# Kernel optimization log

Measured on AMD Instinct MI355X. Metric: run time of the kernel, lower is better.

Reference implementation:

```python
import jax, jax.numpy as jnp
import numpy as np

B, T, QD, AD = 64, 2048, 1024, 256


def setup_inputs() -> dict:
    key = jax.random.key(0)
    k1, k2, k3, k4, k5 = jax.random.split(key, 5)
    encoder_seq_proj = jax.random.normal(k1, (B, T, AD), dtype=jnp.float32)
    query = jax.random.normal(k2, (B, QD), dtype=jnp.float32)
    chars = jax.random.randint(k3, (B, T), 0, 60, dtype=jnp.int64)
    # learned params (nn.Linear, bias=False): weight shape (out, in)
    Wq = jax.random.normal(k4, (AD, QD), dtype=jnp.float32) / np.sqrt(QD)
    v = jax.random.normal(k5, (AD,), dtype=jnp.float32) / np.sqrt(AD)
    return {"encoder_seq_proj": encoder_seq_proj, "query": query,
            "chars": chars, "t": 1, "Wq": Wq, "v": v}


def reference(encoder_seq_proj, query, chars, t, Wq, v):
    # query: (B, QD) -> unsqueeze to (B, 1, QD) is implicit via broadcasting
    processed_query = jnp.einsum('bq,aq->ba', query, Wq)            # (B, AD)
    # broadcast add + tanh + v-reduction (large intermediate (B,T,AD))
    energies = jnp.einsum('bta,a->bt',
                          jnp.tanh(processed_query[:, None, :] + encoder_seq_proj),
                          v)                                          # (B, T)
    energies = energies * (chars != 0).astype(energies.dtype)
    alignment = jax.nn.softmax(energies, axis=1)                     # (B, T)
    return alignment
```

## Files before the change

### kernel.cpp

```cpp
#include <hip/hip_runtime.h>
#include <math.h>

#define BB 64
#define TT 2048
#define QD 1024
#define AD 256

__device__ __forceinline__ float tanh_fast(float x) {
    float e = __expf(2.0f * x);
    return 1.0f - __fdividef(2.0f, e + 1.0f);
}

__global__ __launch_bounds__(256) void pq_kernel(const float* __restrict__ query,
                                                 const float* __restrict__ Wq,
                                                 float* __restrict__ pq) {
    int wg   = (blockIdx.x * blockDim.x + threadIdx.x) >> 6;
    int lane = threadIdx.x & 63;
    int b0 = (wg >> 6) * 4;
    int a0 = (wg & 63) * 4;
    float4 qr[4][4];
    #pragma unroll
    for (int i = 0; i < 4; ++i) {
        const float4* qrow = (const float4*)(query + (size_t)(b0 + i) * QD);
        #pragma unroll
        for (int k = 0; k < 4; ++k) qr[i][k] = qrow[lane + k * 64];
    }
    float acc[4][4];
    #pragma unroll
    for (int j = 0; j < 4; ++j) {
        const float4* wrow = (const float4*)(Wq + (size_t)(a0 + j) * QD);
        float4 w4[4];
        #pragma unroll
        for (int k = 0; k < 4; ++k) w4[k] = wrow[lane + k * 64];
        #pragma unroll
        for (int i = 0; i < 4; ++i) {
            float a = 0.f;
            #pragma unroll
            for (int k = 0; k < 4; ++k)
                a += qr[i][k].x * w4[k].x + qr[i][k].y * w4[k].y
                   + qr[i][k].z * w4[k].z + qr[i][k].w * w4[k].w;
            acc[i][j] = a;
        }
    }
    #pragma unroll
    for (int off = 32; off > 0; off >>= 1)
        #pragma unroll
        for (int i = 0; i < 4; ++i)
            #pragma unroll
            for (int j = 0; j < 4; ++j)
                acc[i][j] += __shfl_down(acc[i][j], off, 64);
    if (lane == 0) {
        #pragma unroll
        for (int i = 0; i < 4; ++i) {
            float4 r = make_float4(acc[i][0], acc[i][1], acc[i][2], acc[i][3]);
            ((float4*)(pq + (size_t)(b0 + i) * AD))[a0 >> 2] = r;
        }
    }
}

__global__ __launch_bounds__(256) void energy_kernel(const float* __restrict__ esp,
                                                     const float* __restrict__ pq,
                                                     const float* __restrict__ v,
                                                     const int* __restrict__ chars,
                                                     float* __restrict__ expout,
                                                     float* __restrict__ partials) {
    __shared__ float red[4];
    int wave = threadIdx.x >> 6;
    int lane = threadIdx.x & 63;
    int wg   = blockIdx.x * 4 + wave;
    int w0 = wg * 4;
    int b  = w0 >> 11;
    const float4* erow = (const float4*)(esp + (size_t)w0 * AD);
    float4 e4[4];
    #pragma unroll
    for (int j = 0; j < 4; ++j) e4[j] = erow[j * 64 + lane];
    float4 p4 = ((const float4*)(pq + (size_t)b * AD))[lane];
    float4 v4 = ((const float4*)v)[lane];
    float s[4];
    #pragma unroll
    for (int j = 0; j < 4; ++j) {
        s[j] = tanh_fast(p4.x + e4[j].x) * v4.x
             + tanh_fast(p4.y + e4[j].y) * v4.y
             + tanh_fast(p4.z + e4[j].z) * v4.z
             + tanh_fast(p4.w + e4[j].w) * v4.w;
    }
    #pragma unroll
    for (int off = 32; off > 0; off >>= 1)
        #pragma unroll
        for (int j = 0; j < 4; ++j)
            s[j] += __shfl_down(s[j], off, 64);
    if (lane == 0) {
        int4 cc = *(const int4*)(chars + w0);
        float4 r;
        r.x = cc.x ? __expf(s[0]) : 1.0f;
        r.y = cc.y ? __expf(s[1]) : 1.0f;
        r.z = cc.z ? __expf(s[2]) : 1.0f;
        r.w = cc.w ? __expf(s[3]) : 1.0f;
        *(float4*)(expout + w0) = r;
        red[wave] = r.x + r.y + r.z + r.w;
    }
    __syncthreads();
    if (threadIdx.x == 0)
        partials[blockIdx.x] = red[0] + red[1] + red[2] + red[3];
}

__global__ __launch_bounds__(1024) void normalize_kernel(float* __restrict__ io,
                                                         const float* __restrict__ partials) {
    __shared__ float red[16];
    int tid  = threadIdx.x;
    int wave = tid >> 6, lane = tid & 63;
    int b = blockIdx.x;
    float p = (tid < 128) ? partials[b * 128 + tid] : 0.0f;
    #pragma unroll
    for (int off = 32; off > 0; off >>= 1)
        p += __shfl_xor(p, off, 64);
    if (lane == 0) red[wave] = p;
    __syncthreads();
    float s = 0.f;
    #pragma unroll
    for (int i = 0; i < 16; ++i) s += red[i];
    float inv = __fdividef(1.0f, s);
    float2* row = (float2*)(io + (size_t)b * TT);
    float2 vv = row[tid];
    row[tid] = make_float2(vv.x * inv, vv.y * inv);
}

extern "C" void kernel_launch(void* const* d_in, const int* in_sizes, int n_in,
                              void* d_out, int out_size, void* d_ws, size_t ws_size,
                              hipStream_t stream) {
    const float* esp   = (const float*)d_in[0];
    const float* query = (const float*)d_in[1];
    const int*   chars = (const int*)d_in[2];
    const float* Wq    = (const float*)d_in[4];
    const float* v     = (const float*)d_in[5];
    float* out = (float*)d_out;
    float* pq       = (float*)d_ws;
    float* partials = (float*)d_ws + BB * AD;

    pq_kernel<<<256, 256, 0, stream>>>(query, Wq, pq);
    energy_kernel<<<(BB * TT) / 16, 256, 0, stream>>>(esp, pq, v, chars, out, partials);
    normalize_kernel<<<BB, 1024, 0, stream>>>(out, partials);
}
```

Baseline: 35.47 us.

## Make energy kernel persistent per row chunk with register double-buffered loads

Each energy block now covers 128 consecutive timesteps of one batch row, looping over 8 chunks and prefetching the next chunk of encoder rows into registers while computing the current one. The grid shrinks from 8192 to 1024 blocks, which amortizes the pq/v loads and cuts per-block overhead, and leaves only 16 partials per row, so normalize sums them in a single thread. The risk is fewer waves in flight to hide memory latency on a bandwidth-bound stream, plus higher register pressure from the double buffer.

```diff
diff --git a/kernel.cpp b/kernel.cpp
--- a/kernel.cpp
+++ b/kernel.cpp
@@ -67,38 +67,57 @@
     __shared__ float red[4];
     int wave = threadIdx.x >> 6;
     int lane = threadIdx.x & 63;
-    int wg   = blockIdx.x * 4 + wave;
-    int w0 = wg * 4;
-    int b  = w0 >> 11;
-    const float4* erow = (const float4*)(esp + (size_t)w0 * AD);
-    float4 e4[4];
-    #pragma unroll
-    for (int j = 0; j < 4; ++j) e4[j] = erow[j * 64 + lane];
+    int b    = blockIdx.x >> 4;
+    int blk  = blockIdx.x & 15;
+    size_t r0 = (size_t)b * TT + blk * 128 + wave * 4;
     float4 p4 = ((const float4*)(pq + (size_t)b * AD))[lane];
     float4 v4 = ((const float4*)v)[lane];
-    float s[4];
-    #pragma unroll
-    for (int j = 0; j < 4; ++j) {
-        s[j] = tanh_fast(p4.x + e4[j].x) * v4.x
-             + tanh_fast(p4.y + e4[j].y) * v4.y
-             + tanh_fast(p4.z + e4[j].z) * v4.z
-             + tanh_fast(p4.w + e4[j].w) * v4.w;
+    float wsum = 0.f;
+
+    float4 cur[4];
+    {
+        const float4* erow = (const float4*)(esp + r0 * AD);
+        #pragma unroll
+        for (int j = 0; j < 4; ++j) cur[j] = erow[j * 64 + lane];
     }
     #pragma unroll
-    for (int off = 32; off > 0; off >>= 1)
+    for (int c = 0; c < 8; ++c) {
+        float4 nxt[4];
+        if (c < 7) {
+            const float4* erow = (const float4*)(esp + (r0 + (size_t)(c + 1) * 16) * AD);
+            #pragma unroll
+            for (int j = 0; j < 4; ++j) nxt[j] = erow[j * 64 + lane];
+        }
+        float s[4];
         #pragma unroll
-        for (int j = 0; j < 4; ++j)
-            s[j] += __shfl_down(s[j], off, 64);
-    if (lane == 0) {
-        int4 cc = *(const int4*)(chars + w0);
-        float4 r;
-        r.x = cc.x ? __expf(s[0]) : 1.0f;
-        r.y = cc.y ? __expf(s[1]) : 1.0f;
-        r.z = cc.z ? __expf(s[2]) : 1.0f;
-        r.w = cc.w ? __expf(s[3]) : 1.0f;
-        *(float4*)(expout + w0) = r;
-        red[wave] = r.x + r.y + r.z + r.w;
+        for (int j = 0; j < 4; ++j) {
+            s[j] = tanh_fast(p4.x + cur[j].x) * v4.x
+                 + tanh_fast(p4.y + cur[j].y) * v4.y
+                 + tanh_fast(p4.z + cur[j].z) * v4.z
+                 + tanh_fast(p4.w + cur[j].w) * v4.w;
+        }
+        #pragma unroll
+        for (int off = 32; off > 0; off >>= 1)
+            #pragma unroll
+            for (int j = 0; j < 4; ++j)
+                s[j] += __shfl_down(s[j], off, 64);
+        if (lane == 0) {
+            size_t w0 = r0 + (size_t)c * 16;
+            int4 cc = *(const int4*)(chars + w0);
+            float4 r;
+            r.x = cc.x ? __expf(s[0]) : 1.0f;
+            r.y = cc.y ? __expf(s[1]) : 1.0f;
+            r.z = cc.z ? __expf(s[2]) : 1.0f;
+            r.w = cc.w ? __expf(s[3]) : 1.0f;
+            *(float4*)(expout + w0) = r;
+            wsum += r.x + r.y + r.z + r.w;
+        }
+        if (c < 7) {
+            #pragma unroll
+            for (int j = 0; j < 4; ++j) cur[j] = nxt[j];
+        }
     }
+    if (lane == 0) red[wave] = wsum;
     __syncthreads();
     if (threadIdx.x == 0)
         partials[blockIdx.x] = red[0] + red[1] + red[2] + red[3];
@@ -106,20 +125,17 @@
 
 __global__ __launch_bounds__(1024) void normalize_kernel(float* __restrict__ io,
                                                          const float* __restrict__ partials) {
-    __shared__ float red[16];
-    int tid  = threadIdx.x;
-    int wave = tid >> 6, lane = tid & 63;
+    __shared__ float sinv;
+    int tid = threadIdx.x;
     int b = blockIdx.x;
-    float p = (tid < 128) ? partials[b * 128 + tid] : 0.0f;
-    #pragma unroll
-    for (int off = 32; off > 0; off >>= 1)
-        p += __shfl_xor(p, off, 64);
-    if (lane == 0) red[wave] = p;
+    if (tid == 0) {
+        float s = 0.f;
+        #pragma unroll
+        for (int i = 0; i < 16; ++i) s += partials[b * 16 + i];
+        sinv = __fdividef(1.0f, s);
+    }
     __syncthreads();
-    float s = 0.f;
-    #pragma unroll
-    for (int i = 0; i < 16; ++i) s += red[i];
-    float inv = __fdividef(1.0f, s);
+    float inv = sinv;
     float2* row = (float2*)(io + (size_t)b * TT);
     float2 vv = row[tid];
     row[tid] = make_float2(vv.x * inv, vv.y * inv);
@@ -138,6 +154,6 @@
     float* partials = (float*)d_ws + BB * AD;
 
     pq_kernel<<<256, 256, 0, stream>>>(query, Wq, pq);
-    energy_kernel<<<(BB * TT) / 16, 256, 0, stream>>>(esp, pq, v, chars, out, partials);
+    energy_kernel<<<1024, 256, 0, stream>>>(esp, pq, v, chars, out, partials);
     normalize_kernel<<<BB, 1024, 0, stream>>>(out, partials);
 }
```

New measurement: 38.33 us. 8.1% more time.

## Process eight rows per wave with transpose-reduce and nontemporal loads

Applied to the files above, without the earlier changes.

Each wave in the energy kernel now handles eight sequence rows instead of four, which halves the grid size. The eight per-row dot products are combined with a butterfly transpose-reduction, so the lanes finish holding different rows' sums instead of every row being fully reduced with shuffles. Encoder loads use nontemporal hints to avoid polluting the cache with streamed data. The normalize kernel reduces 64 partials with one wave and broadcasts the reciprocal through shared memory. The trade-off is more registers per thread and fewer waves to hide memory latency.

```diff
diff --git a/kernel.cpp b/kernel.cpp
--- a/kernel.cpp
+++ b/kernel.cpp
@@ -5,6 +5,8 @@
 #define TT 2048
 #define QD 1024
 #define AD 256
+
+typedef float f32x4 __attribute__((ext_vector_type(4)));
 
 __device__ __forceinline__ float tanh_fast(float x) {
     float e = __expf(2.0f * x);
@@ -68,37 +70,53 @@
     int wave = threadIdx.x >> 6;
     int lane = threadIdx.x & 63;
     int wg   = blockIdx.x * 4 + wave;
-    int w0 = wg * 4;
-    int b  = w0 >> 11;
-    const float4* erow = (const float4*)(esp + (size_t)w0 * AD);
-    float4 e4[4];
-    #pragma unroll
-    for (int j = 0; j < 4; ++j) e4[j] = erow[j * 64 + lane];
+    size_t r0 = (size_t)wg * 8;
+    int b = (int)(r0 >> 11);
     float4 p4 = ((const float4*)(pq + (size_t)b * AD))[lane];
     float4 v4 = ((const float4*)v)[lane];
-    float s[4];
+
+    const f32x4* base = (const f32x4*)(esp + r0 * AD);
+    f32x4 e[8];
     #pragma unroll
-    for (int j = 0; j < 4; ++j) {
-        s[j] = tanh_fast(p4.x + e4[j].x) * v4.x
-             + tanh_fast(p4.y + e4[j].y) * v4.y
-             + tanh_fast(p4.z + e4[j].z) * v4.z
-             + tanh_fast(p4.w + e4[j].w) * v4.w;
+    for (int j = 0; j < 8; ++j)
+        e[j] = __builtin_nontemporal_load(base + j * 64 + lane);
+
+    float s[8];
+    #pragma unroll
+    for (int j = 0; j < 8; ++j) {
+        s[j] = tanh_fast(p4.x + e[j].x) * v4.x
+             + tanh_fast(p4.y + e[j].y) * v4.y
+             + tanh_fast(p4.z + e[j].z) * v4.z
+             + tanh_fast(p4.w + e[j].w) * v4.w;
     }
+
     #pragma unroll
-    for (int off = 32; off > 0; off >>= 1)
+    for (int k = 0; k < 3; ++k) {
+        int m = 4 >> k;
+        int hi = (lane >> k) & 1;
         #pragma unroll
-        for (int j = 0; j < 4; ++j)
-            s[j] += __shfl_down(s[j], off, 64);
-    if (lane == 0) {
-        int4 cc = *(const int4*)(chars + w0);
-        float4 r;
-        r.x = cc.x ? __expf(s[0]) : 1.0f;
-        r.y = cc.y ? __expf(s[1]) : 1.0f;
-        r.z = cc.z ? __expf(s[2]) : 1.0f;
-        r.w = cc.w ? __expf(s[3]) : 1.0f;
-        *(float4*)(expout + w0) = r;
-        red[wave] = r.x + r.y + r.z + r.w;
+        for (int j = 0; j < m; ++j) {
+            float keep = hi ? s[j + m] : s[j];
+            float give = hi ? s[j] : s[j + m];
+            s[j] = keep + __shfl_xor(give, 1 << k, 64);
+        }
     }
+    s[0] += __shfl_xor(s[0], 8, 64);
+    s[0] += __shfl_xor(s[0], 16, 64);
+    s[0] += __shfl_xor(s[0], 32, 64);
+
+    float contrib = 0.f;
+    if (lane < 8) {
+        int row = ((lane & 1) << 2) | (lane & 2) | ((lane >> 2) & 1);
+        int c = chars[r0 + row];
+        float ex = c ? __expf(s[0]) : 1.0f;
+        expout[r0 + row] = ex;
+        contrib = ex;
+    }
+    contrib += __shfl_xor(contrib, 1, 64);
+    contrib += __shfl_xor(contrib, 2, 64);
+    contrib += __shfl_xor(contrib, 4, 64);
+    if (lane == 0) red[wave] = contrib;
     __syncthreads();
     if (threadIdx.x == 0)
         partials[blockIdx.x] = red[0] + red[1] + red[2] + red[3];
@@ -106,20 +124,18 @@
 
 __global__ __launch_bounds__(1024) void normalize_kernel(float* __restrict__ io,
                                                          const float* __restrict__ partials) {
-    __shared__ float red[16];
-    int tid  = threadIdx.x;
-    int wave = tid >> 6, lane = tid & 63;
+    __shared__ float sinv;
+    int tid = threadIdx.x;
     int b = blockIdx.x;
-    float p = (tid < 128) ? partials[b * 128 + tid] : 0.0f;
-    #pragma unroll
-    for (int off = 32; off > 0; off >>= 1)
-        p += __shfl_xor(p, off, 64);
-    if (lane == 0) red[wave] = p;
+    if (tid < 64) {
+        float p = partials[b * 64 + tid];
+        #pragma unroll
+        for (int off = 32; off > 0; off >>= 1)
+            p += __shfl_xor(p, off, 64);
+        if (tid == 0) sinv = __fdividef(1.0f, p);
+    }
     __syncthreads();
-    float s = 0.f;
-    #pragma unroll
-    for (int i = 0; i < 16; ++i) s += red[i];
-    float inv = __fdividef(1.0f, s);
+    float inv = sinv;
     float2* row = (float2*)(io + (size_t)b * TT);
     float2 vv = row[tid];
     row[tid] = make_float2(vv.x * inv, vv.y * inv);
@@ -138,6 +154,6 @@
     float* partials = (float*)d_ws + BB * AD;
 
     pq_kernel<<<256, 256, 0, stream>>>(query, Wq, pq);
-    energy_kernel<<<(BB * TT) / 16, 256, 0, stream>>>(esp, pq, v, chars, out, partials);
+    energy_kernel<<<(BB * TT) / 32, 256, 0, stream>>>(esp, pq, v, chars, out, partials);
     normalize_kernel<<<BB, 1024, 0, stream>>>(out, partials);
 }
```

Result: slower. 38.44 us (+8.4%).
